# Optimization experiments

Measured on AMD Instinct MI355X. Metric: run time of the kernel, lower is better.

Reference implementation:

```python
import jax, jax.numpy as jnp
import numpy as np

B, T, NM = 128, 2048, 8  # batch, nSteps, nMaxwell


def setup_inputs() -> dict:
    key = jax.random.key(0)
    k1, k2, k3 = jax.random.split(key, 3)
    S_e = jax.random.normal(k1, (B, T, 3, 3), dtype=jnp.float32)
    # strictly increasing times per batch element
    dt = jax.random.uniform(k2, (B, T), minval=0.01, maxval=0.1, dtype=jnp.float32)
    t = jnp.cumsum(dt, axis=1)
    # [tau_1..tau_nM, g_infy, g_1..g_nM] -> last dim 2*NM + 1
    PronyParams = jax.random.uniform(k3, (B, T, 2 * NM + 1), minval=0.1, maxval=1.0, dtype=jnp.float32)
    return {"S_e": S_e, "t": t, "PronyParams": PronyParams}


def reference(S_e, t, PronyParams):
    """Viscoelastic 2nd Piola-Kirchhoff stress via recursive Prony update.

    S_e:         [B, T, 3, 3] instantaneous elastic stress
    t:           [B, T] time
    PronyParams: [B, T, 2*nM+1] (relaxation times tau then coefficients g)
    Returns (S, S_infy, Q_sum), each [B, T, 3, 3].
    """
    nM = PronyParams.shape[-1] // 2
    tau = PronyParams[..., :nM]                      # [B,T,nM]
    g = PronyParams[..., nM:]                        # [B,T,nM+1]
    g = g / jnp.sum(g, axis=-1, keepdims=True)
    g_infy = g[..., 0:1]                             # [B,T,1]
    g_i = g[..., 1:]                                 # [B,T,nM]

    Bsz = S_e.shape[0]
    # time-major scan inputs
    xs = (
        jnp.swapaxes(t, 0, 1),      # [T,B]
        jnp.swapaxes(S_e, 0, 1),    # [T,B,3,3]
        jnp.swapaxes(tau, 0, 1),    # [T,B,nM]
        jnp.swapaxes(g_i, 0, 1),    # [T,B,nM]
    )
    init = (
        jnp.zeros((Bsz, nM, 3, 3), S_e.dtype),  # Q_0
        -t[:, 1],                                # t_prev (as in original initializer)
        jnp.zeros((Bsz, 3, 3), S_e.dtype),       # S_prev
        tau[:, 0],
        g_i[:, 0],
    )

    def step(carry, x):
        Q_p, t_p, S_p, tau_p, g_p = carry
        t_c, S_c, tau_c, g_c = x
        g_bar = 0.5 * (g_c + g_p)                 # [B,nM]
        tau_bar = 0.5 * (tau_c + tau_p)           # [B,nM]
        dt = (t_c - t_p)[:, None]                 # [B,1]
        e = jnp.exp(-0.5 * dt / tau_bar)          # exp(-dt/(2 tau_bar))
        term1 = (e * e)[..., None, None]          # exp(-dt/tau_bar), [B,nM,1,1]
        term2 = (e * g_bar)[..., None, None]      # [B,nM,1,1]
        dS = (S_c - S_p)[:, None]                 # [B,1,3,3]
        Q = term1 * Q_p + term2 * dS              # [B,nM,3,3]
        return (Q, t_c, S_c, tau_c, g_c), Q

    _, Qs = jax.lax.scan(step, init, xs)          # [T,B,nM,3,3]
    Q_sum = jnp.swapaxes(jnp.sum(Qs, axis=2), 0, 1)  # [B,T,3,3]
    S_infy = g_infy[..., None] * S_e              # [B,T,1,1] * [B,T,3,3]
    S = S_infy + Q_sum
    return (S, S_infy, Q_sum)
```

## Files before the change

### kernel.cpp

```cpp
#include <hip/hip_runtime.h>

#define T_LEN 2048
#define NMODE 8
#define NPP   17

template <int L, int G>
__global__ __launch_bounds__(256)
void phaseA(const float* __restrict__ Se,
            const float* __restrict__ tt,
            const float* __restrict__ pp,
            float* __restrict__ out,
            float* __restrict__ partR,
            float* __restrict__ partP,
            float* __restrict__ caA,
            int B) {
    constexpr int NC    = T_LEN / L;
    constexpr int NSTEP = G * L;
    constexpr int RW    = NSTEP + 1;
    constexpr int NT    = 256;
    constexpr int RAW_SZ = RW * NPP;
    constexpr int QT_SZ  = 9 * (NSTEP + 4);
    constexpr int CA_K   = L * 8 + 4;
    constexpr int UNION_SZ = (RAW_SZ > QT_SZ + G * CA_K) ? RAW_SZ
                                                         : (QT_SZ + G * CA_K);
    constexpr int AC_K  = L * 16 + 4;
    constexpr int O_AC  = UNION_SZ;
    constexpr int SROW  = NSTEP + 4;
    constexpr int O_ST  = O_AC + G * AC_K;
    constexpr int O_T   = O_ST + 9 * SROW;
    constexpr int O_INV = O_T + RW;
    constexpr int O_GI  = O_INV + RW;
    constexpr int TOTAL = O_GI + RW;

    __shared__ __align__(16) float sm[TOTAL];
    float* s_raw = sm;
    float* s_qT  = sm;
    float* s_ca  = sm + QT_SZ;
    float* s_AC  = sm + O_AC;
    float* s_ST  = sm + O_ST;
    float* s_t   = sm + O_T;
    float* s_inv = sm + O_INV;
    float* s_gi  = sm + O_GI;

    const int tid  = threadIdx.x;
    const int ngrp = NC / G;
    const int b    = blockIdx.x / ngrp;
    const int grp  = blockIdx.x % ngrp;
    const int c0   = grp * G;
    const int base = c0 * L;
    const int off  = (base == 0) ? 0 : 1;
    const int r0   = (base == 0) ? 0 : base - 1;

    {
        const float* pr = pp + ((size_t)b * T_LEN + r0) * NPP;
        for (int i = tid; i < RW * NPP; i += NT) s_raw[i] = pr[i];
        const float* sr = Se + ((size_t)b * T_LEN + r0) * 9;
        for (int i = tid; i < RW * 9; i += NT) {
            int r = i / 9, e = i - r * 9;
            s_ST[e * SROW + r] = sr[i];
        }
        const float* tr = tt + (size_t)b * T_LEN + r0;
        for (int i = tid; i < RW; i += NT) s_t[i] = tr[i];
    }
    __syncthreads();

    for (int i = tid; i < RW; i += NT) {
        float gs = 0.f;
        #pragma unroll
        for (int k = 8; k < NPP; ++k) gs += s_raw[i * NPP + k];
        float iv = __builtin_amdgcn_rcpf(gs);
        s_inv[i] = iv;
        s_gi[i]  = s_raw[i * NPP + 8] * iv;
    }
    __syncthreads();

    for (int i = tid; i < NSTEP * 8; i += NT) {
        int m  = i & 7;
        int ts = i >> 3;
        int rc = ts + off;
        bool first = (base == 0) && (ts == 0);
        int rp = first ? rc : rc - 1;
        float tau_c = s_raw[rc * NPP + m];
        float tau_p = s_raw[rp * NPP + m];
        float gqh_c = 0.5f * s_raw[rc * NPP + 9 + m] * s_inv[rc];
        float gqh_p = 0.5f * s_raw[rp * NPP + 9 + m] * s_inv[rp];
        float t_c = s_t[rc];
        float t_p = first ? -s_t[1] : s_t[rp];
        float ee  = __expf((t_p - t_c) * __builtin_amdgcn_rcpf(tau_c + tau_p));
        int kk = ts / L, sl = ts % L;
        s_AC[kk * AC_K + sl * 16 + m]     = ee * ee;
        s_AC[kk * AC_K + sl * 16 + 8 + m] = ee * (gqh_c + gqh_p);
    }
    __syncthreads();

    const size_t nOut = (size_t)B * T_LEN * 9;

    if (tid < 72) {
        const int k  = tid / 9;
        const int e  = tid - k * 9;
        const int cg = c0 + k;

        float dS[L];
        {
            float Sv[L + 1];
            Sv[0] = (cg == 0) ? 0.f : s_ST[e * SROW + (k * L + off - 1)];
            #pragma unroll
            for (int s = 0; s < L; ++s)
                Sv[s + 1] = s_ST[e * SROW + (k * L + s + off)];
            #pragma unroll
            for (int s = 0; s < L; ++s) dS[s] = Sv[s + 1] - Sv[s];
        }

        float Q[8] = {0,0,0,0,0,0,0,0};
        const float4* acp = (const float4*)(s_AC + k * AC_K);

        float4 a0 = acp[0], a1 = acp[1], c0v = acp[2], c1v = acp[3];
        #pragma unroll
        for (int s = 0; s < L; ++s) {
            float4 na0, na1, nc0, nc1;
            if (s < L - 1) {
                na0 = acp[4*s+4]; na1 = acp[4*s+5];
                nc0 = acp[4*s+6]; nc1 = acp[4*s+7];
            }
            float d = dS[s];
            Q[0] = a0.x*Q[0] + c0v.x*d;  Q[1] = a0.y*Q[1] + c0v.y*d;
            Q[2] = a0.z*Q[2] + c0v.z*d;  Q[3] = a0.w*Q[3] + c0v.w*d;
            Q[4] = a1.x*Q[4] + c1v.x*d;  Q[5] = a1.y*Q[5] + c1v.y*d;
            Q[6] = a1.z*Q[6] + c1v.z*d;  Q[7] = a1.w*Q[7] + c1v.w*d;
            float qs = ((Q[0]+Q[1])+(Q[2]+Q[3])) + ((Q[4]+Q[5])+(Q[6]+Q[7]));
            s_qT[e * SROW + (k * L + s)] = qs;
            a0 = na0; a1 = na1; c0v = nc0; c1v = nc1;
        }

        float4* pr4 = (float4*)(partR + ((size_t)(b * 9 + e) * NC + cg) * 8);
        pr4[0] = make_float4(Q[0], Q[1], Q[2], Q[3]);
        pr4[1] = make_float4(Q[4], Q[5], Q[6], Q[7]);
    } else if (tid < 192) {
        float* o1 = out + nOut + ((size_t)b * T_LEN + base) * 9;
        for (int i = tid - 72; i < NSTEP * 9; i += 120) {
            int t = i / 9, e = i - t * 9;
            int rc = t + off;
            o1[i] = s_gi[rc] * s_ST[e * SROW + rc];
        }
    } else {
        const int u = tid - 192;
        const int k = u >> 3;
        const int m = u & 7;
        float c = 1.f;
        #pragma unroll
        for (int s = 0; s < L; ++s) {
            c *= s_AC[k * AC_K + s * 16 + m];
            s_ca[k * CA_K + s * 8 + m] = c;
        }
        partP[((size_t)b * NC + (c0 + k)) * 8 + m] = c;
    }
    __syncthreads();

    float* o2 = out + 2 * nOut + ((size_t)b * T_LEN + base) * 9;
    for (int i4 = tid; i4 < NSTEP * 9 / 4; i4 += NT) {
        int i = i4 * 4;
        float4 v;
        {
            int t0i = i / 9,     e0i = i - t0i * 9;
            int t1i = (i+1) / 9, e1i = (i+1) - t1i * 9;
            int t2i = (i+2) / 9, e2i = (i+2) - t2i * 9;
            int t3i = (i+3) / 9, e3i = (i+3) - t3i * 9;
            v.x = s_qT[e0i * SROW + t0i];
            v.y = s_qT[e1i * SROW + t1i];
            v.z = s_qT[e2i * SROW + t2i];
            v.w = s_qT[e3i * SROW + t3i];
        }
        ((float4*)o2)[i4] = v;
    }
    float* ca = caA + ((size_t)b * NC + c0) * (L * 8);
    {
        int k = tid >> 5, j = tid & 31;
        const float4* src = (const float4*)(s_ca + k * CA_K);
        ((float4*)(ca + k * L * 8))[j] = src[j];
    }
}

template <int K>
__global__ __launch_bounds__(256)
void chunk_scan_wave(float* __restrict__ R, const float* __restrict__ P,
                     int B) {
    constexpr int NC = K * 64;
    int gtid = blockIdx.x * blockDim.x + threadIdx.x;
    int wid  = gtid >> 6;
    int lane = gtid & 63;
    if (wid >= B * 9) return;
    int e = wid % 9;
    int b = wid / 9;

    float* rp       = R + ((size_t)(b * 9 + e) * NC) * NMODE;
    const float* pq = P + ((size_t)b * NC) * NMODE;

    float pk[K][NMODE], rk[K][NMODE];
    float pa[NMODE], ra[NMODE];
    #pragma unroll
    for (int m = 0; m < NMODE; ++m) { pa[m] = 1.f; ra[m] = 0.f; }

    #pragma unroll
    for (int k = 0; k < K; ++k) {
        int c = lane * K + k;
        const float4* rv = (const float4*)(rp + (size_t)c * NMODE);
        const float4* pv = (const float4*)(pq + (size_t)c * NMODE);
        float4 r0 = rv[0], r1 = rv[1], p0 = pv[0], p1 = pv[1];
        rk[k][0]=r0.x; rk[k][1]=r0.y; rk[k][2]=r0.z; rk[k][3]=r0.w;
        rk[k][4]=r1.x; rk[k][5]=r1.y; rk[k][6]=r1.z; rk[k][7]=r1.w;
        pk[k][0]=p0.x; pk[k][1]=p0.y; pk[k][2]=p0.z; pk[k][3]=p0.w;
        pk[k][4]=p1.x; pk[k][5]=p1.y; pk[k][6]=p1.z; pk[k][7]=p1.w;
        #pragma unroll
        for (int m = 0; m < NMODE; ++m) {
            ra[m] = pk[k][m] * ra[m] + rk[k][m];
            pa[m] = pk[k][m] * pa[m];
        }
    }

    #pragma unroll
    for (int d = 1; d < 64; d <<= 1) {
        #pragma unroll
        for (int m = 0; m < NMODE; ++m) {
            float plo = __shfl_up(pa[m], d);
            float rlo = __shfl_up(ra[m], d);
            if (lane >= d) {
                ra[m] = pa[m] * rlo + ra[m];
                pa[m] = pa[m] * plo;
            }
        }
    }

    float z[NMODE];
    #pragma unroll
    for (int m = 0; m < NMODE; ++m) {
        float zz = __shfl_up(ra[m], 1);
        z[m] = (lane == 0) ? 0.f : zz;
    }

    #pragma unroll
    for (int k = 0; k < K; ++k) {
        int c = lane * K + k;
        float4* rv = (float4*)(rp + (size_t)c * NMODE);
        rv[0] = make_float4(z[0], z[1], z[2], z[3]);
        rv[1] = make_float4(z[4], z[5], z[6], z[7]);
        #pragma unroll
        for (int m = 0; m < NMODE; ++m)
            z[m] = pk[k][m] * z[m] + rk[k][m];
    }
}

template <int L, int GC>
__global__ __launch_bounds__(256)
void phaseC(float* __restrict__ out,
            const float* __restrict__ partR,
            const float* __restrict__ caA,
            int B) {
    constexpr int NC = T_LEN / L;
    constexpr int NE = GC * L * 9;
    const int tid  = threadIdx.x;
    const int ngrp = NC / GC;
    const int b  = blockIdx.x / ngrp;
    const int g  = blockIdx.x % ngrp;
    const int c0 = g * GC;

    __shared__ float s_Z[GC * 72];
    __shared__ __align__(16) float s_ca[GC * L * 8];

    for (int i = tid; i < GC * 72; i += 256) {
        int cl = i / 72, u = i % 72, e = u >> 3, m = u & 7;
        s_Z[i] = partR[((size_t)(b * 9 + e) * NC + c0 + cl) * 8 + m];
    }
    {
        const float4* ca4 = (const float4*)(caA + ((size_t)b * NC + c0) * (L * 8));
        for (int i = tid; i < GC * L * 2; i += 256)
            ((float4*)s_ca)[i] = ca4[i];
    }
    __syncthreads();

    const size_t nOut = (size_t)B * T_LEN * 9;
    float* o = out + ((size_t)b * T_LEN + (size_t)c0 * L) * 9;
    const float4* sf4 = (const float4*)(o + nOut);
    float4* s4 = (float4*)o;
    float4* q4 = (float4*)(o + 2 * nOut);

    for (int i4 = tid; i4 < NE / 4; i4 += 256) {
        int i = i4 * 4;
        float4 qv = q4[i4];
        float4 fv = sf4[i4];
        float corr[4];
        #pragma unroll
        for (int j = 0; j < 4; ++j) {
            int t = (i + j) / 9, e = (i + j) - t * 9;
            int cl = t / L;
            const float* caT = &s_ca[t * 8];
            const float* zE  = &s_Z[cl * 72 + e * 8];
            float cr = 0.f;
            #pragma unroll
            for (int m = 0; m < NMODE; ++m) cr += caT[m] * zE[m];
            corr[j] = cr;
        }
        float4 qn = make_float4(qv.x + corr[0], qv.y + corr[1],
                                qv.z + corr[2], qv.w + corr[3]);
        q4[i4] = qn;
        s4[i4] = make_float4(fv.x + qn.x, fv.y + qn.y,
                             fv.z + qn.z, fv.w + qn.w);
    }
}

extern "C" void kernel_launch(void* const* d_in, const int* in_sizes, int n_in,
                              void* d_out, int out_size, void* d_ws, size_t ws_size,
                              hipStream_t stream) {
    const float* Se = (const float*)d_in[0];
    const float* tt = (const float*)d_in[1];
    const float* pp = (const float*)d_in[2];
    float* out = (float*)d_out;

    int B = in_sizes[1] / T_LEN;

    constexpr int L  = 16;
    constexpr int NC = T_LEN / L;
    constexpr int K  = NC / 64;
    constexpr int G  = 8;
    constexpr int GC = 8;

    float* partR = (float*)d_ws;
    float* partP = partR + (size_t)B * 9 * NC * 8;
    float* caA   = partP + (size_t)B * NC * 8;

    int gridA = B * (NC / G);
    int gridB = (B * 9 * 64 + 255) / 256;
    int gridC = B * (NC / GC);

    phaseA<L, G><<<gridA, dim3(256), 0, stream>>>(
        Se, tt, pp, out, partR, partP, caA, B);
    chunk_scan_wave<K><<<gridB, dim3(256), 0, stream>>>(partR, partP, B);
    phaseC<L, GC><<<gridC, dim3(256), 0, stream>>>(out, partR, caA, B);
}
```

Measured before the change: 108.4 us.

## Store cumulative decay factors in fp16, realign scan threads, use nontemporal stores

The intermediate cumulative-decay array passed from phaseA to phaseC is now stored as fp16 instead of fp32, halving that workspace traffic. The per-chunk scan threads in phaseA are remapped to 16-lane groups (9 active per group), and the gi*S output loop is adjusted to use the remaining 64 threads. phaseC writes its outputs with nontemporal stores. The fp16 storage of decay products loses precision in the correction term, which may exceed tolerance, and the thread remapping idles some lanes.

```diff
diff --git a/kernel.cpp b/kernel.cpp
--- a/kernel.cpp
+++ b/kernel.cpp
@@ -1,8 +1,11 @@
 #include <hip/hip_runtime.h>
+#include <hip/hip_fp16.h>
 
 #define T_LEN 2048
 #define NMODE 8
 #define NPP   17
+
+typedef float floatx4 __attribute__((ext_vector_type(4)));
 
 template <int L, int G>
 __global__ __launch_bounds__(256)
@@ -12,7 +15,7 @@
             float* __restrict__ out,
             float* __restrict__ partR,
             float* __restrict__ partP,
-            float* __restrict__ caA,
+            __half* __restrict__ caA,
             int B) {
     constexpr int NC    = T_LEN / L;
     constexpr int NSTEP = G * L;
@@ -95,49 +98,50 @@
 
     const size_t nOut = (size_t)B * T_LEN * 9;
 
-    if (tid < 72) {
-        const int k  = tid / 9;
-        const int e  = tid - k * 9;
-        const int cg = c0 + k;
-
-        float dS[L];
-        {
-            float Sv[L + 1];
-            Sv[0] = (cg == 0) ? 0.f : s_ST[e * SROW + (k * L + off - 1)];
+    if (tid < 128) {
+        const int k = tid >> 4;
+        const int e = tid & 15;
+        if (e < 9) {
+            const int cg = c0 + k;
+            float dS[L];
+            {
+                float Sv[L + 1];
+                Sv[0] = (cg == 0) ? 0.f : s_ST[e * SROW + (k * L + off - 1)];
+                #pragma unroll
+                for (int s = 0; s < L; ++s)
+                    Sv[s + 1] = s_ST[e * SROW + (k * L + s + off)];
+                #pragma unroll
+                for (int s = 0; s < L; ++s) dS[s] = Sv[s + 1] - Sv[s];
+            }
+
+            float Q[8] = {0,0,0,0,0,0,0,0};
+            const float4* acp = (const float4*)(s_AC + k * AC_K);
+
+            float4 a0 = acp[0], a1 = acp[1], c0v = acp[2], c1v = acp[3];
             #pragma unroll
-            for (int s = 0; s < L; ++s)
-                Sv[s + 1] = s_ST[e * SROW + (k * L + s + off)];
-            #pragma unroll
-            for (int s = 0; s < L; ++s) dS[s] = Sv[s + 1] - Sv[s];
-        }
-
-        float Q[8] = {0,0,0,0,0,0,0,0};
-        const float4* acp = (const float4*)(s_AC + k * AC_K);
-
-        float4 a0 = acp[0], a1 = acp[1], c0v = acp[2], c1v = acp[3];
-        #pragma unroll
-        for (int s = 0; s < L; ++s) {
-            float4 na0, na1, nc0, nc1;
-            if (s < L - 1) {
-                na0 = acp[4*s+4]; na1 = acp[4*s+5];
-                nc0 = acp[4*s+6]; nc1 = acp[4*s+7];
+            for (int s = 0; s < L; ++s) {
+                float4 na0, na1, nc0, nc1;
+                if (s < L - 1) {
+                    na0 = acp[4*s+4]; na1 = acp[4*s+5];
+                    nc0 = acp[4*s+6]; nc1 = acp[4*s+7];
+                }
+                float d = dS[s];
+                Q[0] = a0.x*Q[0] + c0v.x*d;  Q[1] = a0.y*Q[1] + c0v.y*d;
+                Q[2] = a0.z*Q[2] + c0v.z*d;  Q[3] = a0.w*Q[3] + c0v.w*d;
+                Q[4] = a1.x*Q[4] + c1v.x*d;  Q[5] = a1.y*Q[5] + c1v.y*d;
+                Q[6] = a1.z*Q[6] + c1v.z*d;  Q[7] = a1.w*Q[7] + c1v.w*d;
+                float qs = ((Q[0]+Q[1])+(Q[2]+Q[3])) + ((Q[4]+Q[5])+(Q[6]+Q[7]));
+                s_qT[e * SROW + (k * L + s)] = qs;
+                a0 = na0; a1 = na1; c0v = nc0; c1v = nc1;
             }
-            float d = dS[s];
-            Q[0] = a0.x*Q[0] + c0v.x*d;  Q[1] = a0.y*Q[1] + c0v.y*d;
-            Q[2] = a0.z*Q[2] + c0v.z*d;  Q[3] = a0.w*Q[3] + c0v.w*d;
-            Q[4] = a1.x*Q[4] + c1v.x*d;  Q[5] = a1.y*Q[5] + c1v.y*d;
-            Q[6] = a1.z*Q[6] + c1v.z*d;  Q[7] = a1.w*Q[7] + c1v.w*d;
-            float qs = ((Q[0]+Q[1])+(Q[2]+Q[3])) + ((Q[4]+Q[5])+(Q[6]+Q[7]));
-            s_qT[e * SROW + (k * L + s)] = qs;
-            a0 = na0; a1 = na1; c0v = nc0; c1v = nc1;
-        }
-
-        float4* pr4 = (float4*)(partR + ((size_t)(b * 9 + e) * NC + cg) * 8);
-        pr4[0] = make_float4(Q[0], Q[1], Q[2], Q[3]);
-        pr4[1] = make_float4(Q[4], Q[5], Q[6], Q[7]);
+
+            float4* pr4 = (float4*)(partR + ((size_t)(b * 9 + e) * NC + cg) * 8);
+            pr4[0] = make_float4(Q[0], Q[1], Q[2], Q[3]);
+            pr4[1] = make_float4(Q[4], Q[5], Q[6], Q[7]);
+        }
     } else if (tid < 192) {
         float* o1 = out + nOut + ((size_t)b * T_LEN + base) * 9;
-        for (int i = tid - 72; i < NSTEP * 9; i += 120) {
+        for (int i = tid - 128; i < NSTEP * 9; i += 64) {
             int t = i / 9, e = i - t * 9;
             int rc = t + off;
             o1[i] = s_gi[rc] * s_ST[e * SROW + rc];
@@ -172,11 +176,17 @@
         }
         ((float4*)o2)[i4] = v;
     }
-    float* ca = caA + ((size_t)b * NC + c0) * (L * 8);
     {
-        int k = tid >> 5, j = tid & 31;
-        const float4* src = (const float4*)(s_ca + k * CA_K);
-        ((float4*)(ca + k * L * 8))[j] = src[j];
+        __half2* ca2 = (__half2*)(caA + ((size_t)b * NC + c0) * (L * 8));
+        for (int j = tid; j < G * L * 8 / 2; j += NT) {
+            int h = 2 * j;
+            int k = h >> 7;
+            int r = h & 127;
+            int s = r >> 3, m = r & 7;
+            float va = s_ca[k * CA_K + s * 8 + m];
+            float vb = s_ca[k * CA_K + s * 8 + m + 1];
+            ca2[j] = __float22half2_rn(make_float2(va, vb));
+        }
     }
 }
 
@@ -253,7 +263,7 @@
 __global__ __launch_bounds__(256)
 void phaseC(float* __restrict__ out,
             const float* __restrict__ partR,
-            const float* __restrict__ caA,
+            const __half* __restrict__ caA,
             int B) {
     constexpr int NC = T_LEN / L;
     constexpr int NE = GC * L * 9;
@@ -271,21 +281,24 @@
         s_Z[i] = partR[((size_t)(b * 9 + e) * NC + c0 + cl) * 8 + m];
     }
     {
-        const float4* ca4 = (const float4*)(caA + ((size_t)b * NC + c0) * (L * 8));
-        for (int i = tid; i < GC * L * 2; i += 256)
-            ((float4*)s_ca)[i] = ca4[i];
+        const __half2* ca2 = (const __half2*)(caA + ((size_t)b * NC + c0) * (L * 8));
+        for (int i = tid; i < GC * L * 4; i += 256) {
+            float2 v = __half22float2(ca2[i]);
+            s_ca[2 * i]     = v.x;
+            s_ca[2 * i + 1] = v.y;
+        }
     }
     __syncthreads();
 
     const size_t nOut = (size_t)B * T_LEN * 9;
     float* o = out + ((size_t)b * T_LEN + (size_t)c0 * L) * 9;
     const float4* sf4 = (const float4*)(o + nOut);
-    float4* s4 = (float4*)o;
-    float4* q4 = (float4*)(o + 2 * nOut);
+    floatx4* s4 = (floatx4*)o;
+    floatx4* q4 = (floatx4*)(o + 2 * nOut);
 
     for (int i4 = tid; i4 < NE / 4; i4 += 256) {
         int i = i4 * 4;
-        float4 qv = q4[i4];
+        floatx4 qv = q4[i4];
         float4 fv = sf4[i4];
         float corr[4];
         #pragma unroll
@@ -299,11 +312,14 @@
             for (int m = 0; m < NMODE; ++m) cr += caT[m] * zE[m];
             corr[j] = cr;
         }
-        float4 qn = make_float4(qv.x + corr[0], qv.y + corr[1],
-                                qv.z + corr[2], qv.w + corr[3]);
-        q4[i4] = qn;
-        s4[i4] = make_float4(fv.x + qn.x, fv.y + qn.y,
-                             fv.z + qn.z, fv.w + qn.w);
+        floatx4 qn;
+        qn.x = qv.x + corr[0]; qn.y = qv.y + corr[1];
+        qn.z = qv.z + corr[2]; qn.w = qv.w + corr[3];
+        floatx4 sn;
+        sn.x = fv.x + qn.x; sn.y = fv.y + qn.y;
+        sn.z = fv.z + qn.z; sn.w = fv.w + qn.w;
+        __builtin_nontemporal_store(qn, &q4[i4]);
+        __builtin_nontemporal_store(sn, &s4[i4]);
     }
 }
 
@@ -323,9 +339,9 @@
     constexpr int G  = 8;
     constexpr int GC = 8;
 
-    float* partR = (float*)d_ws;
-    float* partP = partR + (size_t)B * 9 * NC * 8;
-    float* caA   = partP + (size_t)B * NC * 8;
+    float*  partR = (float*)d_ws;
+    float*  partP = partR + (size_t)B * 9 * NC * 8;
+    __half* caA   = (__half*)(partP + (size_t)B * NC * 8);
 
     int gridA = B * (NC / G);
     int gridB = (B * 9 * 64 + 255) / 256;
```

After: 110.5 us. No clear change (+1.9%).
